# Kernel tuning notes

Hardware: AMD Instinct MI355X
Metric: run time of the kernel (lower is better)

The kernel has to match this reference:

```python
import jax, jax.numpy as jnp
import numpy as np

DIM = 768
NUM_HEADS = 12
HEAD_DIM = DIM // NUM_HEADS
SCALE = HEAD_DIM ** -0.5


def setup_inputs() -> dict:
    key = jax.random.key(0)
    k_x, k_qkv, k_pw, k_pb = jax.random.split(key, 4)
    B, N = 2, 4096
    x = jax.random.normal(k_x, (B, N, DIM), dtype=jnp.float32)
    # Linear weights stored as [in, out] for x @ W
    w_qkv = jax.random.normal(k_qkv, (DIM, 3 * DIM), dtype=jnp.float32) * (DIM ** -0.5)
    w_proj = jax.random.normal(k_pw, (DIM, DIM), dtype=jnp.float32) * (DIM ** -0.5)
    b_proj = jax.random.normal(k_pb, (DIM,), dtype=jnp.float32) * 0.02
    return {"x": x, "w_qkv": w_qkv, "w_proj": w_proj, "b_proj": b_proj}


def reference(x, w_qkv, w_proj, b_proj):
    B, N, D = x.shape
    H, Hd = NUM_HEADS, HEAD_DIM
    qkv = (x @ w_qkv).reshape(B, N, 3, H, Hd)
    qkv = jnp.transpose(qkv, (2, 0, 3, 1, 4))  # [3, B, H, N, Hd]
    q, k, v = qkv[0], qkv[1], qkv[2]
    attn = jnp.einsum("bhnd,bhmd->bhnm", q, k) * SCALE  # [B,H,N,N]
    attn = jax.nn.softmax(attn, axis=-1)
    out = jnp.einsum("bhnm,bhmd->bhnd", attn, v)  # [B,H,N,Hd]
    out = jnp.transpose(out, (0, 2, 1, 3)).reshape(B, N, D)
    return out @ w_proj + b_proj
```

## Files before the change

### kernel.cpp

```cpp
#include <hip/hip_runtime.h>
#include <hip/hip_bf16.h>


#define NSEQ 4096
#define NTOK 8192
#define NHD  12
#define QSCALE 0.18033688011112043f

typedef __attribute__((ext_vector_type(8)))  __bf16 bf16x8;
typedef __attribute__((ext_vector_type(4)))  __bf16 bf16x4;
typedef __attribute__((ext_vector_type(2)))  __bf16 bf16x2;
typedef __attribute__((ext_vector_type(8)))  unsigned short u16x8;
typedef __attribute__((ext_vector_type(4)))  float  f32x4;
typedef __attribute__((ext_vector_type(16))) float  f32x16;

typedef const __attribute__((address_space(1))) unsigned int* as1_u32p;
typedef __attribute__((address_space(3))) unsigned int*       as3_u32p;

#if defined(__has_builtin)
#  if __has_builtin(__builtin_amdgcn_exp2f)
#    define EXP2(x) __builtin_amdgcn_exp2f(x)
#  else
#    define EXP2(x) exp2f(x)
#  endif
#else
#  define EXP2(x) exp2f(x)
#endif

__device__ inline f32x4 mfma16(bf16x8 a, bf16x8 b, f32x4 c) {
    return __builtin_amdgcn_mfma_f32_16x16x32_bf16(a, b, c, 0, 0, 0);
}
__device__ inline f32x16 mfma32(bf16x8 a, bf16x8 b, f32x16 c) {
    return __builtin_amdgcn_mfma_f32_32x32x16_bf16(a, b, c, 0, 0, 0);
}

__device__ inline unsigned int pack2(float x, float y) {
    union { bf16x2 v; unsigned int u; } c;
    c.v[0] = (__bf16)x; c.v[1] = (__bf16)y;
    return c.u;
}

__device__ __forceinline__ void gload16(const __bf16* g, __bf16* l) {
    __builtin_amdgcn_global_load_lds((as1_u32p)g, (as3_u32p)l, 16, 0, 0);
}

__global__ __launch_bounds__(256)
void cvt_bf16_kernel(const float* __restrict__ x, __bf16* __restrict__ y)
{
    const size_t i = ((size_t)blockIdx.x * 256 + threadIdx.x) * 8;
    f32x4 a = *(const f32x4*)(x + i);
    f32x4 b = *(const f32x4*)(x + i + 4);
    bf16x8 w;
    #pragma unroll
    for (int j = 0; j < 4; ++j) { w[j] = (__bf16)a[j]; w[4 + j] = (__bf16)b[j]; }
    *(bf16x8*)(y + i) = w;
}

__global__ __launch_bounds__(256)
void wT_kernel(const float* __restrict__ W, __bf16* __restrict__ WT, int K, int N)
{
    __shared__ float t[32][33];
    const int tid = threadIdx.x;
    const int bk = blockIdx.x * 32, bn = blockIdx.y * 32;
    const int tx = tid & 31, ty = tid >> 5;
    #pragma unroll
    for (int i = 0; i < 4; ++i)
        t[ty + 8 * i][tx] = W[(size_t)(bk + ty + 8 * i) * N + bn + tx];
    __syncthreads();
    const int n = bn + (tid >> 3), kc = (tid & 7) * 4;
    bf16x4 w;
    #pragma unroll
    for (int j = 0; j < 4; ++j) w[j] = (__bf16)t[kc + j][tid >> 3];
    *(bf16x4*)(WT + (size_t)n * K + bk + kc) = w;
}

template<int EPI>
__global__ __launch_bounds__(256)
void gemm_kernel(const __bf16* __restrict__ A, const __bf16* __restrict__ BT,
                 const float* __restrict__ bias, void* __restrict__ Cp,
                 int M, int N, int K)
{
    __shared__ __bf16 lds_a[128 * 32];
    __shared__ __bf16 lds_b[128 * 32];
    const int tid  = threadIdx.x;
    const int lane = tid & 63, wave = tid >> 6;
    const int l16  = lane & 15, lg = lane >> 4;
    const int wr = (wave >> 1) * 64, wc = (wave & 1) * 64;
    const int m0 = blockIdx.x * 128, n0 = blockIdx.y * 128;

    f32x4 acc[4][4] = {};

    for (int k0 = 0; k0 < K; k0 += 32) {
        #pragma unroll
        for (int i = 0; i < 2; ++i) {
            const int s   = i * 256 + tid;
            const int row = s >> 2, ch = s & 3;
            __bf16* la = lds_a + (i * 256 + wave * 64) * 8;
            __bf16* lb = lds_b + (i * 256 + wave * 64) * 8;
            gload16(A  + (size_t)(m0 + row) * K + k0 + ch * 8, la);
            gload16(BT + (size_t)(n0 + row) * K + k0 + ch * 8, lb);
        }
        __syncthreads();

        bf16x8 a[4], b[4];
        #pragma unroll
        for (int mf = 0; mf < 4; ++mf)
            a[mf] = *(const bf16x8*)&lds_a[(wr + mf * 16 + l16) * 32 + lg * 8];
        #pragma unroll
        for (int nf = 0; nf < 4; ++nf)
            b[nf] = *(const bf16x8*)&lds_b[(wc + nf * 16 + l16) * 32 + lg * 8];
        __builtin_amdgcn_s_setprio(1);
        #pragma unroll
        for (int mf = 0; mf < 4; ++mf)
            #pragma unroll
            for (int nf = 0; nf < 4; ++nf)
                acc[mf][nf] = mfma16(a[mf], b[nf], acc[mf][nf]);
        __builtin_amdgcn_s_setprio(0);
        __syncthreads();
    }

    #pragma unroll
    for (int mf = 0; mf < 4; ++mf) {
        #pragma unroll
        for (int nf = 0; nf < 4; ++nf) {
            int n = n0 + wc + nf * 16 + l16;
            #pragma unroll
            for (int r = 0; r < 4; ++r) {
                int m = m0 + wr + mf * 16 + lg * 4 + r;
                float v = acc[mf][nf][r];
                if constexpr (EPI == 0) {
                    if (n < 768) v *= QSCALE;
                    ((__bf16*)Cp)[(size_t)m * N + n] = (__bf16)v;
                } else {
                    ((float*)Cp)[(size_t)m * N + n] = v + bias[n];
                }
            }
        }
    }
}

__global__ __launch_bounds__(256, 3)
void attn_kernel(const __bf16* __restrict__ qkv, __bf16* __restrict__ out)
{
    __shared__ __bf16 k_lds[2][64 * 72];
    __shared__ __bf16 v_lds[2][64 * 64];

    const int tid = threadIdx.x, lane = tid & 63, wave = tid >> 6;
    const int l31 = lane & 31, hi = lane >> 5;
    const bool hib = (hi != 0);

    int bid = (blockIdx.x & 7) * 96 + (blockIdx.x >> 3);
    const int qt = bid & 31;
    const int h  = (bid >> 5) % NHD;
    const int b  = bid / (32 * NHD);
    const size_t rowbase = (size_t)b * NSEQ;
    const int q = qt * 128 + wave * 32 + l31;

    bf16x8 qf[4];
    #pragma unroll
    for (int ks = 0; ks < 4; ++ks)
        qf[ks] = *(const bf16x8*)(qkv + (rowbase + q) * 2304 + h * 64 + ks * 16 + hi * 8);

    f32x16 o[2] = {};
    float l_r = 0.f;

    const int krow = tid >> 3, kq = tid & 7;
    const int vt   = tid >> 3, vq = tid & 7;
    u16x8 kreg0, kreg1, vreg0, vreg1;

    auto load_kv = [&](int kt) {
        const unsigned short* q16 = (const unsigned short*)qkv;
        size_t base = rowbase + (size_t)kt * 64;
        kreg0 = *(const u16x8*)(q16 + (base + krow)       * 2304 + 768  + h * 64 + kq * 8);
        kreg1 = *(const u16x8*)(q16 + (base + krow + 32)  * 2304 + 768  + h * 64 + kq * 8);
        vreg0 = *(const u16x8*)(q16 + (base + 2 * vt)     * 2304 + 1536 + h * 64 + vq * 8);
        vreg1 = *(const u16x8*)(q16 + (base + 2 * vt + 1) * 2304 + 1536 + h * 64 + vq * 8);
    };
    auto store_kv = [&](int bsel) {
        *(u16x8*)&k_lds[bsel][krow * 72 + kq * 8]        = kreg0;
        *(u16x8*)&k_lds[bsel][(krow + 32) * 72 + kq * 8] = kreg1;
        #pragma unroll
        for (int j = 0; j < 8; ++j) {
            int d = vq * 8 + j;
            int chunk = ((vt >> 2) ^ d ^ (d >> 3)) & 7;
            unsigned int val = (unsigned int)vreg0[j] | ((unsigned int)vreg1[j] << 16);
            *(unsigned int*)((char*)&v_lds[bsel][0] + d * 128 + chunk * 16 + (vt & 3) * 4) = val;
        }
    };

    load_kv(0);
    store_kv(0);
    __syncthreads();

    const int NT = NSEQ / 64;
    for (int kt = 0; kt < NT; ++kt) {
        const int cur = kt & 1;
        if (kt + 1 < NT) load_kv(kt + 1);

        f32x16 sc[2] = {};
        __builtin_amdgcn_s_setprio(1);
        #pragma unroll
        for (int tb = 0; tb < 2; ++tb) {
            #pragma unroll
            for (int ks = 0; ks < 4; ++ks) {
                bf16x8 kf = *(const bf16x8*)&k_lds[cur][(tb * 32 + l31) * 72 + ks * 16 + hi * 8];
                sc[tb] = mfma32(kf, qf[ks], sc[tb]);
            }
        }
        __builtin_amdgcn_s_setprio(0);

        unsigned int pk0[2][4], pk1[2][4];
        float rs = 0.f;
        #pragma unroll
        for (int tb = 0; tb < 2; ++tb) {
            #pragma unroll
            for (int g = 0; g < 4; ++g) {
                float p0 = EXP2(sc[tb][4 * g + 0]);
                float p1 = EXP2(sc[tb][4 * g + 1]);
                float p2 = EXP2(sc[tb][4 * g + 2]);
                float p3 = EXP2(sc[tb][4 * g + 3]);
                rs += (p0 + p1) + (p2 + p3);
                pk0[tb][g] = pack2(p0, p1);
                pk1[tb][g] = pack2(p2, p3);
            }
        }
        l_r += rs;

        __builtin_amdgcn_s_setprio(1);
        #pragma unroll
        for (int ks = 0; ks < 4; ++ks) {
            const int tb = ks >> 1, gL = 2 * (ks & 1), gH = gL + 1;
            unsigned int pL0 = pk0[tb][gL], pL1 = pk1[tb][gL];
            unsigned int pH0 = pk0[tb][gH], pH1 = pk1[tb][gH];
            unsigned int rL0 = (unsigned int)__shfl_xor((int)pL0, 32);
            unsigned int rL1 = (unsigned int)__shfl_xor((int)pL1, 32);
            unsigned int rH0 = (unsigned int)__shfl_xor((int)pH0, 32);
            unsigned int rH1 = (unsigned int)__shfl_xor((int)pH1, 32);
            union { bf16x8 v; unsigned int u[4]; } pf;
            pf.u[0] = hib ? rH0 : pL0;
            pf.u[1] = hib ? rH1 : pL1;
            pf.u[2] = hib ? pH0 : rL0;
            pf.u[3] = hib ? pH1 : rL1;
            #pragma unroll
            for (int db = 0; db < 2; ++db) {
                int d = db * 32 + l31;
                int chunk = ((2 * ks + hi) ^ d ^ (d >> 3)) & 7;
                bf16x8 vf = *(const bf16x8*)((const char*)&v_lds[cur][0] + d * 128 + chunk * 16);
                o[db] = mfma32(vf, pf.v, o[db]);
            }
        }
        __builtin_amdgcn_s_setprio(0);

        if (kt + 1 < NT) store_kv(cur ^ 1);
        __syncthreads();
    }

    l_r += __shfl_xor(l_r, 32);
    float inv = 1.0f / l_r;
    size_t row = rowbase + q;
    #pragma unroll
    for (int db = 0; db < 2; ++db) {
        #pragma unroll
        for (int rr = 0; rr < 4; ++rr) {
            int d0 = db * 32 + rr * 8 + hi * 4;
            bf16x4 w;
            #pragma unroll
            for (int i = 0; i < 4; ++i) w[i] = (__bf16)(o[db][4 * rr + i] * inv);
            *(bf16x4*)(out + row * 768 + h * 64 + d0) = w;
        }
    }
}

extern "C" void kernel_launch(void* const* d_in, const int* in_sizes, int n_in,
                              void* d_out, int out_size, void* d_ws, size_t ws_size,
                              hipStream_t stream)
{
    const float* x      = (const float*)d_in[0];
    const float* w_qkv  = (const float*)d_in[1];
    const float* w_proj = (const float*)d_in[2];
    const float* b_proj = (const float*)d_in[3];
    float* out = (float*)d_out;

    __bf16* qkv    = (__bf16*)d_ws;
    __bf16* attn   = qkv + (size_t)NTOK * 2304;
    __bf16* wqkvT  = attn;
    __bf16* wprojT = attn + (size_t)NTOK * 768;
    __bf16* x_bf16 = (__bf16*)d_out;

    cvt_bf16_kernel<<<dim3(NTOK * 768 / (256 * 8)), 256, 0, stream>>>(x, x_bf16);
    wT_kernel<<<dim3(24, 72), 256, 0, stream>>>(w_qkv, wqkvT, 768, 2304);
    wT_kernel<<<dim3(24, 24), 256, 0, stream>>>(w_proj, wprojT, 768, 768);

    gemm_kernel<0><<<dim3(64, 18), 256, 0, stream>>>(x_bf16, wqkvT, nullptr, qkv,
                                                     NTOK, 3 * 768, 768);
    attn_kernel<<<dim3(2 * NHD * 32), 256, 0, stream>>>(qkv, attn);
    gemm_kernel<1><<<dim3(64, 6), 256, 0, stream>>>(attn, wprojT, b_proj, out,
                                                    NTOK, 768, 768);
}
```

Baseline: 286.5 us.

## Fuse fp32-to-bf16 input conversion into QKV GEMM and use permlane32 swap

Drops the separate x conversion kernel. The QKV GEMM now loads fp32 rows of x into registers, converts them to bf16 and stores them into padded LDS, with the next tile prefetched in registers. This removes one kernel launch and a round trip of the converted x through memory, but the QKV GEMM now reads twice as many bytes for A and does the conversion on the critical path. Separately, the attention P-fragment exchange replaces four shuffles and selects with two v_permlane32_swap instructions.

```diff
diff --git a/kernel.cpp b/kernel.cpp
--- a/kernel.cpp
+++ b/kernel.cpp
@@ -40,20 +40,12 @@
     return c.u;
 }
 
+__device__ __forceinline__ void permswap(unsigned int& a, unsigned int& b) {
+    asm volatile("v_permlane32_swap_b32 %0, %1" : "+v"(a), "+v"(b));
+}
+
 __device__ __forceinline__ void gload16(const __bf16* g, __bf16* l) {
     __builtin_amdgcn_global_load_lds((as1_u32p)g, (as3_u32p)l, 16, 0, 0);
-}
-
-__global__ __launch_bounds__(256)
-void cvt_bf16_kernel(const float* __restrict__ x, __bf16* __restrict__ y)
-{
-    const size_t i = ((size_t)blockIdx.x * 256 + threadIdx.x) * 8;
-    f32x4 a = *(const f32x4*)(x + i);
-    f32x4 b = *(const f32x4*)(x + i + 4);
-    bf16x8 w;
-    #pragma unroll
-    for (int j = 0; j < 4; ++j) { w[j] = (__bf16)a[j]; w[4 + j] = (__bf16)b[j]; }
-    *(bf16x8*)(y + i) = w;
 }
 
 __global__ __launch_bounds__(256)
@@ -74,13 +66,14 @@
     *(bf16x4*)(WT + (size_t)n * K + bk + kc) = w;
 }
 
-template<int EPI>
+template<int A_F32, int EPI>
 __global__ __launch_bounds__(256)
-void gemm_kernel(const __bf16* __restrict__ A, const __bf16* __restrict__ BT,
+void gemm_kernel(const void* __restrict__ Ap, const __bf16* __restrict__ BT,
                  const float* __restrict__ bias, void* __restrict__ Cp,
                  int M, int N, int K)
 {
-    __shared__ __bf16 lds_a[128 * 32];
+    constexpr int AST = A_F32 ? 36 : 32;
+    __shared__ __bf16 lds_a[128 * AST];
     __shared__ __bf16 lds_b[128 * 32];
     const int tid  = threadIdx.x;
     const int lane = tid & 63, wave = tid >> 6;
@@ -88,24 +81,48 @@
     const int wr = (wave >> 1) * 64, wc = (wave & 1) * 64;
     const int m0 = blockIdx.x * 128, n0 = blockIdx.y * 128;
 
+    const int ar8 = tid >> 3, aq8 = tid & 7;
+    f32x4 areg[4];
+
+    auto load_a = [&](int k0) {
+        const float* A = (const float*)Ap;
+        #pragma unroll
+        for (int i = 0; i < 4; ++i)
+            areg[i] = *(const f32x4*)(A + (size_t)(m0 + ar8 + i * 32) * K + k0 + aq8 * 4);
+    };
+    auto store_a = [&]() {
+        #pragma unroll
+        for (int i = 0; i < 4; ++i) {
+            bf16x4 w;
+            #pragma unroll
+            for (int c = 0; c < 4; ++c) w[c] = (__bf16)areg[i][c];
+            *(bf16x4*)&lds_a[(ar8 + i * 32) * AST + aq8 * 4] = w;
+        }
+    };
+
     f32x4 acc[4][4] = {};
+    if constexpr (A_F32) load_a(0);
 
     for (int k0 = 0; k0 < K; k0 += 32) {
         #pragma unroll
         for (int i = 0; i < 2; ++i) {
             const int s   = i * 256 + tid;
             const int row = s >> 2, ch = s & 3;
-            __bf16* la = lds_a + (i * 256 + wave * 64) * 8;
             __bf16* lb = lds_b + (i * 256 + wave * 64) * 8;
-            gload16(A  + (size_t)(m0 + row) * K + k0 + ch * 8, la);
             gload16(BT + (size_t)(n0 + row) * K + k0 + ch * 8, lb);
-        }
+            if constexpr (!A_F32) {
+                __bf16* la = lds_a + (i * 256 + wave * 64) * 8;
+                gload16((const __bf16*)Ap + (size_t)(m0 + row) * K + k0 + ch * 8, la);
+            }
+        }
+        if constexpr (A_F32) store_a();
         __syncthreads();
+        if constexpr (A_F32) { if (k0 + 32 < K) load_a(k0 + 32); }
 
         bf16x8 a[4], b[4];
         #pragma unroll
         for (int mf = 0; mf < 4; ++mf)
-            a[mf] = *(const bf16x8*)&lds_a[(wr + mf * 16 + l16) * 32 + lg * 8];
+            a[mf] = *(const bf16x8*)&lds_a[(wr + mf * 16 + l16) * AST + lg * 8];
         #pragma unroll
         for (int nf = 0; nf < 4; ++nf)
             b[nf] = *(const bf16x8*)&lds_b[(wc + nf * 16 + l16) * 32 + lg * 8];
@@ -147,7 +164,6 @@
 
     const int tid = threadIdx.x, lane = tid & 63, wave = tid >> 6;
     const int l31 = lane & 31, hi = lane >> 5;
-    const bool hib = (hi != 0);
 
     int bid = (blockIdx.x & 7) * 96 + (blockIdx.x >> 3);
     const int qt = bid & 31;
@@ -230,17 +246,12 @@
         #pragma unroll
         for (int ks = 0; ks < 4; ++ks) {
             const int tb = ks >> 1, gL = 2 * (ks & 1), gH = gL + 1;
-            unsigned int pL0 = pk0[tb][gL], pL1 = pk1[tb][gL];
-            unsigned int pH0 = pk0[tb][gH], pH1 = pk1[tb][gH];
-            unsigned int rL0 = (unsigned int)__shfl_xor((int)pL0, 32);
-            unsigned int rL1 = (unsigned int)__shfl_xor((int)pL1, 32);
-            unsigned int rH0 = (unsigned int)__shfl_xor((int)pH0, 32);
-            unsigned int rH1 = (unsigned int)__shfl_xor((int)pH1, 32);
+            unsigned int u0 = pk0[tb][gL], u2 = pk0[tb][gH];
+            unsigned int u1 = pk1[tb][gL], u3 = pk1[tb][gH];
+            permswap(u0, u2);
+            permswap(u1, u3);
             union { bf16x8 v; unsigned int u[4]; } pf;
-            pf.u[0] = hib ? rH0 : pL0;
-            pf.u[1] = hib ? rH1 : pL1;
-            pf.u[2] = hib ? pH0 : rL0;
-            pf.u[3] = hib ? pH1 : rL1;
+            pf.u[0] = u0; pf.u[1] = u1; pf.u[2] = u2; pf.u[3] = u3;
             #pragma unroll
             for (int db = 0; db < 2; ++db) {
                 int d = db * 32 + l31;
@@ -285,15 +296,13 @@
     __bf16* attn   = qkv + (size_t)NTOK * 2304;
     __bf16* wqkvT  = attn;
     __bf16* wprojT = attn + (size_t)NTOK * 768;
-    __bf16* x_bf16 = (__bf16*)d_out;
-
-    cvt_bf16_kernel<<<dim3(NTOK * 768 / (256 * 8)), 256, 0, stream>>>(x, x_bf16);
+
     wT_kernel<<<dim3(24, 72), 256, 0, stream>>>(w_qkv, wqkvT, 768, 2304);
     wT_kernel<<<dim3(24, 24), 256, 0, stream>>>(w_proj, wprojT, 768, 768);
 
-    gemm_kernel<0><<<dim3(64, 18), 256, 0, stream>>>(x_bf16, wqkvT, nullptr, qkv,
-                                                     NTOK, 3 * 768, 768);
+    gemm_kernel<1, 0><<<dim3(64, 18), 256, 0, stream>>>(x, wqkvT, nullptr, qkv,
+                                                        NTOK, 3 * 768, 768);
     attn_kernel<<<dim3(2 * NHD * 32), 256, 0, stream>>>(qkv, attn);
-    gemm_kernel<1><<<dim3(64, 6), 256, 0, stream>>>(attn, wprojT, b_proj, out,
-                                                    NTOK, 768, 768);
-}
+    gemm_kernel<0, 1><<<dim3(64, 6), 256, 0, stream>>>(attn, wprojT, b_proj, out,
+                                                       NTOK, 768, 768);
+}
```

New measurement: 276.2 us. 3.6% less time.
